# Optimization experiments

Hardware: AMD Instinct MI355X
Metric: run time of the kernel (lower is better)

The kernel has to match this reference:

```python
import jax, jax.numpy as jnp
import numpy as np

N = 10000   # nodes
E = 320000  # directed edges (self-loops added inside reference, per PyG default)
H1, C = 4, 128  # gat1: 4 heads x 128; gat2: 1 head x 128
NEG_SLOPE = 0.2


def _glorot(k, shape):
    lim = float(np.sqrt(6.0 / (shape[0] + shape[-1])))
    return jax.random.uniform(k, shape, jnp.float32, -lim, lim)


def setup_inputs() -> dict:
    key = jax.random.key(0)
    ks = jax.random.split(key, 12)
    x = jax.random.normal(ks[0], (N, 2), jnp.float32)
    edge_index = jax.random.randint(ks[1], (2, E), 0, N, dtype=jnp.int32).astype(jnp.int64)
    W1 = _glorot(ks[2], (2, H1 * C))
    att_src1 = _glorot(ks[3], (H1, C))
    att_dst1 = _glorot(ks[4], (H1, C))
    b1 = jnp.zeros((H1 * C,), jnp.float32)
    W2 = _glorot(ks[5], (H1 * C, C))
    att_src2 = _glorot(ks[6], (1, C))
    att_dst2 = _glorot(ks[7], (1, C))
    b2 = jnp.zeros((C,), jnp.float32)
    Wp = _glorot(ks[8], (C, 1))
    bp = jnp.zeros((1,), jnp.float32)
    return dict(x=x, edge_index=edge_index, W1=W1, att_src1=att_src1, att_dst1=att_dst1,
                b1=b1, W2=W2, att_src2=att_src2, att_dst2=att_dst2, b2=b2, Wp=Wp, bp=bp)


def _gat_conv(x, src, dst, W, a_src, a_dst, b, heads, ch, concat):
    n = x.shape[0]
    h = (x @ W).reshape(n, heads, ch)                         # [N,H,C]
    # per-node attention halves, gathered per edge
    e = jax.nn.leaky_relu((h * a_src).sum(-1)[src] + (h * a_dst).sum(-1)[dst],
                          NEG_SLOPE)                           # [E,H]
    # segment softmax over incoming edges of each destination node
    m = jax.ops.segment_max(e, dst, num_segments=n)            # [N,H]
    p = jnp.exp(e - m[dst])
    s = jax.ops.segment_sum(p, dst, num_segments=n)
    alpha = p / (s[dst] + 1e-16)                               # [E,H]
    out = jax.ops.segment_sum(h[src] * alpha[..., None], dst, num_segments=n)  # [N,H,C]
    out = out.reshape(n, heads * ch) if concat else out.mean(axis=1)
    return out + b


def reference(x, edge_index, W1, att_src1, att_dst1, b1, W2, att_src2, att_dst2, b2, Wp, bp):
    n = x.shape[0]
    loop = jnp.arange(n, dtype=edge_index.dtype)               # PyG add_self_loops=True
    src = jnp.concatenate([edge_index[0], loop])
    dst = jnp.concatenate([edge_index[1], loop])
    h = jax.nn.relu(_gat_conv(x, src, dst, W1, att_src1, att_dst1, b1, H1, C, True))
    h = jax.nn.relu(_gat_conv(h, src, dst, W2, att_src2, att_dst2, b2, 1, C, True))
    logits = h @ Wp + bp                                       # [N,1]
    return logits.squeeze(-1)
```

## Files before the change

### kernel.cpp

```cpp
#include <hip/hip_runtime.h>
#include <hip/hip_fp16.h>
#include <math.h>

#define N_NODES 10000
#define E_IN    320000
#define E_TOT   330000
#define H1      4
#define C       128
#define F1      512

typedef _Float16 f16x8 __attribute__((ext_vector_type(8)));
typedef float    f32x4 __attribute__((ext_vector_type(4)));

__global__ __launch_bounds__(256) void k_as1z(
    const float* __restrict__ x, const float* __restrict__ W1,
    const float* __restrict__ asw, const float* __restrict__ adw,
    float4* __restrict__ as1v, float4* __restrict__ ad1v, int* __restrict__ deg)
{
    __shared__ float red[4][8];
    __shared__ float prep_s[16];
    int tid = threadIdx.x;
    {
        int j = tid;
        int j2 = tid + 256;
        float w0a = W1[j],  w1a = W1[F1 + j];
        float w0b = W1[j2], w1b = W1[F1 + j2];
        float aa = asw[j], dd = adw[j], ab = asw[j2], db = adw[j2];
        float q0 = w0a*aa, q1 = w1a*aa, q2 = w0a*dd, q3 = w1a*dd;
        float q4 = w0b*ab, q5 = w1b*ab, q6 = w0b*db, q7 = w1b*db;
        #pragma unroll
        for (int o = 32; o > 0; o >>= 1) {
            q0 += __shfl_down(q0, o); q1 += __shfl_down(q1, o);
            q2 += __shfl_down(q2, o); q3 += __shfl_down(q3, o);
            q4 += __shfl_down(q4, o); q5 += __shfl_down(q5, o);
            q6 += __shfl_down(q6, o); q7 += __shfl_down(q7, o);
        }
        int wave = tid >> 6, lane = tid & 63;
        if (lane == 0) {
            red[wave][0] = q0; red[wave][1] = q1; red[wave][2] = q2; red[wave][3] = q3;
            red[wave][4] = q4; red[wave][5] = q5; red[wave][6] = q6; red[wave][7] = q7;
        }
        __syncthreads();
        if (tid < 16) {
            int t = tid >> 2;
            int h = tid & 3;
            int w0 = (h & 1) * 2;
            int r  = t + (h >> 1) * 4;
            prep_s[t*4 + h] = red[w0][r] + red[w0+1][r];
        }
        __syncthreads();
    }
    int n = blockIdx.x * 256 + tid;
    if (n >= N_NODES) return;
    deg[n] = 0;
    float x0 = x[2*n], x1 = x[2*n+1];
    float4 A0 = *(const float4*)(prep_s);
    float4 A1 = *(const float4*)(prep_s + 4);
    float4 D0 = *(const float4*)(prep_s + 8);
    float4 D1 = *(const float4*)(prep_s + 12);
    as1v[n] = make_float4(x0*A0.x + x1*A1.x, x0*A0.y + x1*A1.y,
                          x0*A0.z + x1*A1.z, x0*A0.w + x1*A1.w);
    ad1v[n] = make_float4(x0*D0.x + x1*D1.x, x0*D0.y + x1*D1.y,
                          x0*D0.z + x1*D1.z, x0*D0.w + x1*D1.w);
}

__global__ __launch_bounds__(256) void k_w2cvt(
    const float* __restrict__ W2, _Float16* __restrict__ w2h)
{
    int t = blockIdx.x * 256 + threadIdx.x;
    int e0 = t * 4;
    int c = e0 >> 9;
    int kk0 = e0 & 511;
    int xr = (c & 7) << 3;
    _Float16 o[4];
    #pragma unroll
    for (int j = 0; j < 4; ++j) {
        int k = (kk0 + j) ^ xr;
        o[j] = (_Float16)W2[k * C + c];
    }
    *(uint2*)(w2h + c * F1 + kk0) = *(uint2*)o;
}

__global__ void k_hist(const int* __restrict__ dsti, int* __restrict__ deg) {
    int t = blockIdx.x * blockDim.x + threadIdx.x;
    if (t >= E_TOT) return;
    int d = (t < E_IN) ? dsti[t] : (t - E_IN);
    atomicAdd(&deg[d], 1);
}

__global__ __launch_bounds__(256) void k_scan(
    const int* __restrict__ deg, int* __restrict__ offs, int* __restrict__ cursor)
{
    __shared__ int part[256];
    int tid = threadIdx.x;
    const int CH = (N_NODES + 255) / 256;
    int start = tid * CH;
    int sum = 0;
    for (int i = 0; i < CH; ++i) { int idx = start + i; if (idx < N_NODES) sum += deg[idx]; }
    part[tid] = sum;
    __syncthreads();
    for (int off = 1; off < 256; off <<= 1) {
        int v = (tid >= off) ? part[tid - off] : 0;
        __syncthreads();
        part[tid] += v;
        __syncthreads();
    }
    int base = (tid == 0) ? 0 : part[tid - 1];
    for (int i = 0; i < CH; ++i) {
        int idx = start + i;
        if (idx < N_NODES) { offs[idx] = base; cursor[idx] = base; base += deg[idx]; }
    }
    if (tid == 255) offs[N_NODES] = base;
}

__global__ void k_scatter(const int* __restrict__ srci, const int* __restrict__ dsti,
                          int* __restrict__ cursor, int* __restrict__ scsr) {
    int t = blockIdx.x * blockDim.x + threadIdx.x;
    if (t >= E_TOT) return;
    int d = (t < E_IN) ? dsti[t] : (t - E_IN);
    int s = (t < E_IN) ? srci[t] : (t - E_IN);
    int pos = atomicAdd(&cursor[d], 1);
    scsr[pos] = s;
}

__global__ __launch_bounds__(256) void k_fused1(
    const int* __restrict__ offs, const int* __restrict__ scsr,
    const float4* __restrict__ as1v, const float4* __restrict__ ad1v,
    const float2* __restrict__ xv, float* __restrict__ wxn)
{
    int node = blockIdx.x * 16 + (threadIdx.x >> 4);
    int sub = threadIdx.x & 15;
    int beg = offs[node], end = offs[node + 1];
    float4 ad = ad1v[node];
    float s0 = 0.f, s1 = 0.f, s2 = 0.f, s3 = 0.f;
    float w00 = 0.f, w01 = 0.f, w10 = 0.f, w11 = 0.f;
    float w20 = 0.f, w21 = 0.f, w30 = 0.f, w31 = 0.f;
    int i = beg + sub;
    if (i < end) {
        int s = scsr[i];
        for (;;) {
            float4 a = as1v[s];
            float2 xs = xv[s];
            int inext = i + 16;
            bool more = inext < end;
            int snext = 0;
            if (more) snext = scsr[inext];
            float e0 = a.x + ad.x; e0 = e0 > 0.f ? e0 : 0.2f*e0;
            float e1 = a.y + ad.y; e1 = e1 > 0.f ? e1 : 0.2f*e1;
            float e2 = a.z + ad.z; e2 = e2 > 0.f ? e2 : 0.2f*e2;
            float e3 = a.w + ad.w; e3 = e3 > 0.f ? e3 : 0.2f*e3;
            float p0 = __expf(e0), p1 = __expf(e1), p2 = __expf(e2), p3 = __expf(e3);
            s0 += p0; s1 += p1; s2 += p2; s3 += p3;
            w00 += p0*xs.x; w01 += p0*xs.y; w10 += p1*xs.x; w11 += p1*xs.y;
            w20 += p2*xs.x; w21 += p2*xs.y; w30 += p3*xs.x; w31 += p3*xs.y;
            if (!more) break;
            i = inext; s = snext;
        }
    }
    #pragma unroll
    for (int o = 1; o < 16; o <<= 1) {
        s0 += __shfl_xor(s0, o); s1 += __shfl_xor(s1, o);
        s2 += __shfl_xor(s2, o); s3 += __shfl_xor(s3, o);
        w00 += __shfl_xor(w00, o); w01 += __shfl_xor(w01, o);
        w10 += __shfl_xor(w10, o); w11 += __shfl_xor(w11, o);
        w20 += __shfl_xor(w20, o); w21 += __shfl_xor(w21, o);
        w30 += __shfl_xor(w30, o); w31 += __shfl_xor(w31, o);
    }
    if (sub == 0) {
        float i0 = 1.f/(s0 + 1e-16f), i1 = 1.f/(s1 + 1e-16f);
        float i2 = 1.f/(s2 + 1e-16f), i3 = 1.f/(s3 + 1e-16f);
        float4* W = (float4*)(wxn + node*8);
        W[0] = make_float4(w00*i0, w01*i0, w10*i1, w11*i1);
        W[1] = make_float4(w20*i2, w21*i2, w30*i3, w31*i3);
    }
}

__global__ __launch_bounds__(256, 1) void k_gemm2(
    const float* __restrict__ wxn, const float* __restrict__ W1,
    const float* __restrict__ b1, const _Float16* __restrict__ w2h,
    const float* __restrict__ asw, const float* __restrict__ adw,
    __half* __restrict__ h2h, float* __restrict__ as2, float* __restrict__ ad2)
{
    __shared__ _Float16 w2t[F1 * C];
    int tid = threadIdx.x;
    #pragma unroll
    for (int it = 0; it < 32; ++it) {
        int idx = (it * 256 + tid) * 8;
        *(f16x8*)(w2t + idx) = *(const f16x8*)(w2h + idx);
    }
    __syncthreads();

    int wid = tid >> 6, lane = tid & 63;
    int tile = blockIdx.x * 4 + wid;
    if (tile >= N_NODES / 16) return;
    int n0w = tile * 16;
    int col = lane & 15;
    int krow = (lane >> 4) * 8;
    int qr4 = (lane >> 4) * 4;
    int node = n0w + col;

    float4 wv0 = *(const float4*)(wxn + node * 8);
    float4 wv1 = *(const float4*)(wxn + node * 8 + 4);

    f32x4 acc[8];
    #pragma unroll
    for (int mt = 0; mt < 8; ++mt) acc[mt] = (f32x4){0.f, 0.f, 0.f, 0.f};

    int xr = (col & 7) << 3;
    const float* W1r0 = W1;
    const float* W1r1 = W1 + F1;

    #pragma unroll
    for (int h = 0; h < 4; ++h) {
        float wa = (h == 0) ? wv0.x : (h == 1) ? wv0.z : (h == 2) ? wv1.x : wv1.z;
        float wb = (h == 0) ? wv0.y : (h == 1) ? wv0.w : (h == 2) ? wv1.y : wv1.w;
        #pragma unroll
        for (int kq = 0; kq < 4; ++kq) {
            int kc = h * 4 + kq;
            int k0 = kc * 32 + krow;
            float4 a0 = *(const float4*)(W1r0 + k0);
            float4 a1 = *(const float4*)(W1r0 + k0 + 4);
            float4 c0 = *(const float4*)(W1r1 + k0);
            float4 c1 = *(const float4*)(W1r1 + k0 + 4);
            float4 b0 = *(const float4*)(b1 + k0);
            float4 b1v = *(const float4*)(b1 + k0 + 4);
            f16x8 bf;
            float v;
            v = wa*a0.x + wb*c0.x + b0.x;  bf[0] = (_Float16)(v > 0.f ? v : 0.f);
            v = wa*a0.y + wb*c0.y + b0.y;  bf[1] = (_Float16)(v > 0.f ? v : 0.f);
            v = wa*a0.z + wb*c0.z + b0.z;  bf[2] = (_Float16)(v > 0.f ? v : 0.f);
            v = wa*a0.w + wb*c0.w + b0.w;  bf[3] = (_Float16)(v > 0.f ? v : 0.f);
            v = wa*a1.x + wb*c1.x + b1v.x; bf[4] = (_Float16)(v > 0.f ? v : 0.f);
            v = wa*a1.y + wb*c1.y + b1v.y; bf[5] = (_Float16)(v > 0.f ? v : 0.f);
            v = wa*a1.z + wb*c1.z + b1v.z; bf[6] = (_Float16)(v > 0.f ? v : 0.f);
            v = wa*a1.w + wb*c1.w + b1v.w; bf[7] = (_Float16)(v > 0.f ? v : 0.f);
            int kbase = col * F1 + (k0 ^ xr);
            #pragma unroll
            for (int mt = 0; mt < 8; ++mt) {
                f16x8 af = *(const f16x8*)(&w2t[mt * 16 * F1 + kbase]);
                acc[mt] = __builtin_amdgcn_mfma_f32_16x16x32_f16(af, bf, acc[mt], 0, 0, 0);
            }
        }
    }

    float ps = 0.f, pd = 0.f;
    __half* hbase = h2h + (size_t)node * C + qr4;
    #pragma unroll
    for (int mt = 0; mt < 8; ++mt) {
        f32x4 a = acc[mt];
        __half2 lo = __floats2half2_rn(a[0], a[1]);
        __half2 hi = __floats2half2_rn(a[2], a[3]);
        uint2 u; u.x = *(uint*)&lo; u.y = *(uint*)&hi;
        *(uint2*)(hbase + mt * 16) = u;
        float4 av = *(const float4*)(asw + mt * 16 + qr4);
        float4 dv = *(const float4*)(adw + mt * 16 + qr4);
        ps += a[0]*av.x + a[1]*av.y + a[2]*av.z + a[3]*av.w;
        pd += a[0]*dv.x + a[1]*dv.y + a[2]*dv.z + a[3]*dv.w;
    }
    ps += __shfl_xor(ps, 16); ps += __shfl_xor(ps, 32);
    pd += __shfl_xor(pd, 16); pd += __shfl_xor(pd, 32);
    if (lane < 16) { as2[n0w + lane] = ps; ad2[n0w + lane] = pd; }
}

__global__ __launch_bounds__(256) void k_agg2(
    const int* __restrict__ offs, const int* __restrict__ scsr,
    const float* __restrict__ as2, const float* __restrict__ ad2,
    const __half* __restrict__ h2h, const float* __restrict__ b2,
    const float* __restrict__ Wp, const float* __restrict__ bp,
    float* __restrict__ out)
{
    int n = blockIdx.x * 4 + (threadIdx.x >> 6);
    int lane = threadIdx.x & 63;
    int half = lane >> 5;
    int cl = lane & 31;
    int beg = offs[n], end = offs[n + 1];
    float adn = ad2[n];
    float a0 = 0.f, a1 = 0.f, a2 = 0.f, a3 = 0.f, psum = 0.f;
    int i = beg + half;
    for (; i + 6 < end; i += 8) {
        int s0 = scsr[i], s1 = scsr[i+2], s2 = scsr[i+4], s3 = scsr[i+6];
        float e0 = as2[s0] + adn, e1 = as2[s1] + adn;
        float e2 = as2[s2] + adn, e3 = as2[s3] + adn;
        uint2 q0 = *(const uint2*)(h2h + (size_t)s0*C + 4*cl);
        uint2 q1 = *(const uint2*)(h2h + (size_t)s1*C + 4*cl);
        uint2 q2 = *(const uint2*)(h2h + (size_t)s2*C + 4*cl);
        uint2 q3 = *(const uint2*)(h2h + (size_t)s3*C + 4*cl);
        e0 = e0 > 0.f ? e0 : 0.2f*e0;  float p0 = __expf(e0);
        e1 = e1 > 0.f ? e1 : 0.2f*e1;  float p1 = __expf(e1);
        e2 = e2 > 0.f ? e2 : 0.2f*e2;  float p2 = __expf(e2);
        e3 = e3 > 0.f ? e3 : 0.2f*e3;  float p3 = __expf(e3);
        psum += (p0 + p1) + (p2 + p3);
        float2 f0a = __half22float2(*(__half2*)&q0.x), f0b = __half22float2(*(__half2*)&q0.y);
        float2 f1a = __half22float2(*(__half2*)&q1.x), f1b = __half22float2(*(__half2*)&q1.y);
        float2 f2a = __half22float2(*(__half2*)&q2.x), f2b = __half22float2(*(__half2*)&q2.y);
        float2 f3a = __half22float2(*(__half2*)&q3.x), f3b = __half22float2(*(__half2*)&q3.y);
        a0 += p0*f0a.x + p1*f1a.x + p2*f2a.x + p3*f3a.x;
        a1 += p0*f0a.y + p1*f1a.y + p2*f2a.y + p3*f3a.y;
        a2 += p0*f0b.x + p1*f1b.x + p2*f2b.x + p3*f3b.x;
        a3 += p0*f0b.y + p1*f1b.y + p2*f2b.y + p3*f3b.y;
    }
    for (; i < end; i += 2) {
        int s = scsr[i];
        float e = as2[s] + adn; e = e > 0.f ? e : 0.2f*e;
        float p = __expf(e);
        psum += p;
        uint2 q = *(const uint2*)(h2h + (size_t)s*C + 4*cl);
        float2 fa = __half22float2(*(__half2*)&q.x), fb = __half22float2(*(__half2*)&q.y);
        a0 += p*fa.x; a1 += p*fa.y; a2 += p*fb.x; a3 += p*fb.y;
    }
    a0 += __shfl_xor(a0, 32); a1 += __shfl_xor(a1, 32);
    a2 += __shfl_xor(a2, 32); a3 += __shfl_xor(a3, 32);
    psum += __shfl_xor(psum, 32);
    float inv = 1.f / (psum + 1e-16f);
    float4 bb = *(const float4*)(b2 + 4*cl);
    float4 wp = *(const float4*)(Wp + 4*cl);
    float v0 = a0*inv + bb.x; v0 = v0 > 0.f ? v0 : 0.f;
    float v1 = a1*inv + bb.y; v1 = v1 > 0.f ? v1 : 0.f;
    float v2 = a2*inv + bb.z; v2 = v2 > 0.f ? v2 : 0.f;
    float v3 = a3*inv + bb.w; v3 = v3 > 0.f ? v3 : 0.f;
    float contrib = v0*wp.x + v1*wp.y + v2*wp.z + v3*wp.w;
    #pragma unroll
    for (int o = 1; o < 32; o <<= 1) contrib += __shfl_xor(contrib, o);
    if (lane == 0) out[n] = contrib + bp[0];
}

extern "C" void kernel_launch(void* const* d_in, const int* in_sizes, int n_in,
                              void* d_out, int out_size, void* d_ws, size_t ws_size,
                              hipStream_t stream)
{
    const float* x    = (const float*)d_in[0];
    const int*   ei   = (const int*)d_in[1];
    const int*   srci = ei;
    const int*   dsti = ei + E_IN;
    const float* W1   = (const float*)d_in[2];
    const float* as1w = (const float*)d_in[3];
    const float* ad1w = (const float*)d_in[4];
    const float* b1   = (const float*)d_in[5];
    const float* W2   = (const float*)d_in[6];
    const float* as2w = (const float*)d_in[7];
    const float* ad2w = (const float*)d_in[8];
    const float* b2   = (const float*)d_in[9];
    const float* Wp   = (const float*)d_in[10];
    const float* bp   = (const float*)d_in[11];
    float* out = (float*)d_out;

    char* ws = (char*)d_ws;
    size_t off = 0;
    auto alloc = [&](size_t bytes) -> char* {
        char* p = ws + off;
        off = (off + bytes + 255) & ~(size_t)255;
        return p;
    };
    float4*    as1v   = (float4*)alloc((size_t)N_NODES * 16);
    float4*    ad1v   = (float4*)alloc((size_t)N_NODES * 16);
    float*     wxn    = (float*)alloc((size_t)N_NODES * 8 * 4);
    __half*    h2h    = (__half*)alloc((size_t)N_NODES * C * 2);
    _Float16*  w2h    = (_Float16*)alloc((size_t)F1 * C * 2);
    float*     as2    = (float*)alloc((size_t)N_NODES * 4);
    float*     ad2    = (float*)alloc((size_t)N_NODES * 4);
    int*       deg    = (int*)alloc((size_t)N_NODES * 4);
    int*       offs   = (int*)alloc((size_t)(N_NODES + 1) * 4);
    int*       cursor = (int*)alloc((size_t)N_NODES * 4);
    int*       scsr   = (int*)alloc((size_t)E_TOT * 4);

    const int EB = 256;
    const int egrid = (E_TOT + EB - 1) / EB;
    const int ngrid = (N_NODES + 255) / 256;

    k_as1z<<<ngrid, 256, 0, stream>>>(x, W1, as1w, ad1w, as1v, ad1v, deg);
    k_w2cvt<<<64, 256, 0, stream>>>(W2, w2h);
    k_hist<<<egrid, EB, 0, stream>>>(dsti, deg);
    k_scan<<<1, 256, 0, stream>>>(deg, offs, cursor);
    k_scatter<<<egrid, EB, 0, stream>>>(srci, dsti, cursor, scsr);
    k_fused1<<<N_NODES / 16, 256, 0, stream>>>(offs, scsr, as1v, ad1v,
                                               (const float2*)x, wxn);
    k_gemm2<<<(N_NODES/16 + 3) / 4, 256, 0, stream>>>(wxn, W1, b1, w2h, as2w, ad2w,
                                                      h2h, as2, ad2);
    k_agg2<<<N_NODES / 4, 256, 0, stream>>>(offs, scsr, as2, ad2, h2h, b2, Wp, bp, out);
}
```

Measured before the change: 185.8 us.

## Fuse CSR build and layer-1 aggregation into one cooperative persistent kernel

Replaces six separate launches (prep, W2 convert, histogram, scan, scatter, layer-1 aggregate) with a single cooperative kernel of 512 blocks that separates the phases with grid.sync(). The single-block scan becomes a two-level parallel scan: 40 blocks each scan their chunk, then one thread combines the block sums. The aim is to cut kernel launch overhead and the serial scan bottleneck. In exchange it adds six grid-wide barriers, and the grid-stride loops run on a fixed 512-block grid that depends on cooperative residency.

```diff
diff --git a/kernel.cpp b/kernel.cpp
--- a/kernel.cpp
+++ b/kernel.cpp
@@ -1,6 +1,9 @@
 #include <hip/hip_runtime.h>
+#include <hip/hip_cooperative_groups.h>
 #include <hip/hip_fp16.h>
 #include <math.h>
+
+namespace cg = cooperative_groups;
 
 #define N_NODES 10000
 #define E_IN    320000
@@ -8,21 +11,29 @@
 #define H1      4
 #define C       128
 #define F1      512
+#define GB      512
 
 typedef _Float16 f16x8 __attribute__((ext_vector_type(8)));
 typedef float    f32x4 __attribute__((ext_vector_type(4)));
 
-__global__ __launch_bounds__(256) void k_as1z(
-    const float* __restrict__ x, const float* __restrict__ W1,
-    const float* __restrict__ asw, const float* __restrict__ adw,
-    float4* __restrict__ as1v, float4* __restrict__ ad1v, int* __restrict__ deg)
+__global__ __launch_bounds__(256, 2) void k_build(
+    const float* __restrict__ x, const int* __restrict__ srci, const int* __restrict__ dsti,
+    const float* __restrict__ W1, const float* __restrict__ asw, const float* __restrict__ adw,
+    const float* __restrict__ W2, _Float16* __restrict__ w2h,
+    float4* __restrict__ as1v, float4* __restrict__ ad1v,
+    int* __restrict__ deg, int* __restrict__ offs, int* __restrict__ cursor,
+    int* __restrict__ scsr, int* __restrict__ exclg, int* __restrict__ bsum,
+    float* __restrict__ wxn)
 {
+    cg::grid_group grid = cg::this_grid();
     __shared__ float red[4][8];
     __shared__ float prep_s[16];
+    __shared__ int sc[256];
     int tid = threadIdx.x;
-    {
-        int j = tid;
-        int j2 = tid + 256;
+    int b = blockIdx.x;
+
+    if (b < 40) {
+        int j = tid, j2 = tid + 256;
         float w0a = W1[j],  w1a = W1[F1 + j];
         float w0b = W1[j2], w1b = W1[F1 + j2];
         float aa = asw[j], dd = adw[j], ab = asw[j2], db = adw[j2];
@@ -49,129 +60,122 @@
             prep_s[t*4 + h] = red[w0][r] + red[w0+1][r];
         }
         __syncthreads();
-    }
-    int n = blockIdx.x * 256 + tid;
-    if (n >= N_NODES) return;
-    deg[n] = 0;
-    float x0 = x[2*n], x1 = x[2*n+1];
-    float4 A0 = *(const float4*)(prep_s);
-    float4 A1 = *(const float4*)(prep_s + 4);
-    float4 D0 = *(const float4*)(prep_s + 8);
-    float4 D1 = *(const float4*)(prep_s + 12);
-    as1v[n] = make_float4(x0*A0.x + x1*A1.x, x0*A0.y + x1*A1.y,
-                          x0*A0.z + x1*A1.z, x0*A0.w + x1*A1.w);
-    ad1v[n] = make_float4(x0*D0.x + x1*D1.x, x0*D0.y + x1*D1.y,
-                          x0*D0.z + x1*D1.z, x0*D0.w + x1*D1.w);
-}
-
-__global__ __launch_bounds__(256) void k_w2cvt(
-    const float* __restrict__ W2, _Float16* __restrict__ w2h)
-{
-    int t = blockIdx.x * 256 + threadIdx.x;
-    int e0 = t * 4;
-    int c = e0 >> 9;
-    int kk0 = e0 & 511;
-    int xr = (c & 7) << 3;
-    _Float16 o[4];
-    #pragma unroll
-    for (int j = 0; j < 4; ++j) {
-        int k = (kk0 + j) ^ xr;
-        o[j] = (_Float16)W2[k * C + c];
-    }
-    *(uint2*)(w2h + c * F1 + kk0) = *(uint2*)o;
-}
-
-__global__ void k_hist(const int* __restrict__ dsti, int* __restrict__ deg) {
-    int t = blockIdx.x * blockDim.x + threadIdx.x;
-    if (t >= E_TOT) return;
-    int d = (t < E_IN) ? dsti[t] : (t - E_IN);
-    atomicAdd(&deg[d], 1);
-}
-
-__global__ __launch_bounds__(256) void k_scan(
-    const int* __restrict__ deg, int* __restrict__ offs, int* __restrict__ cursor)
-{
-    __shared__ int part[256];
-    int tid = threadIdx.x;
-    const int CH = (N_NODES + 255) / 256;
-    int start = tid * CH;
-    int sum = 0;
-    for (int i = 0; i < CH; ++i) { int idx = start + i; if (idx < N_NODES) sum += deg[idx]; }
-    part[tid] = sum;
-    __syncthreads();
-    for (int off = 1; off < 256; off <<= 1) {
-        int v = (tid >= off) ? part[tid - off] : 0;
+        int n = b * 256 + tid;
+        if (n < N_NODES) {
+            deg[n] = 0;
+            float x0 = x[2*n], x1 = x[2*n+1];
+            float4 A0 = *(const float4*)(prep_s);
+            float4 A1 = *(const float4*)(prep_s + 4);
+            float4 D0 = *(const float4*)(prep_s + 8);
+            float4 D1 = *(const float4*)(prep_s + 12);
+            as1v[n] = make_float4(x0*A0.x + x1*A1.x, x0*A0.y + x1*A1.y,
+                                  x0*A0.z + x1*A1.z, x0*A0.w + x1*A1.w);
+            ad1v[n] = make_float4(x0*D0.x + x1*D1.x, x0*D0.y + x1*D1.y,
+                                  x0*D0.z + x1*D1.z, x0*D0.w + x1*D1.w);
+        }
+    } else if (b < 104) {
+        int t = (b - 40) * 256 + tid;
+        int e0 = t * 4;
+        int c = e0 >> 9;
+        int kk0 = e0 & 511;
+        int xr = (c & 7) << 3;
+        _Float16 o4[4];
+        #pragma unroll
+        for (int j = 0; j < 4; ++j) o4[j] = (_Float16)W2[((kk0 + j) ^ xr) * C + c];
+        *(uint2*)(w2h + c * F1 + kk0) = *(uint2*)o4;
+    }
+    grid.sync();
+
+    for (int t = b * 256 + tid; t < E_TOT; t += GB * 256) {
+        int d = (t < E_IN) ? dsti[t] : (t - E_IN);
+        atomicAdd(&deg[d], 1);
+    }
+    grid.sync();
+
+    int n2 = b * 256 + tid;
+    if (b < 40) {
+        int v = (n2 < N_NODES) ? deg[n2] : 0;
+        sc[tid] = v;
         __syncthreads();
-        part[tid] += v;
-        __syncthreads();
-    }
-    int base = (tid == 0) ? 0 : part[tid - 1];
-    for (int i = 0; i < CH; ++i) {
-        int idx = start + i;
-        if (idx < N_NODES) { offs[idx] = base; cursor[idx] = base; base += deg[idx]; }
-    }
-    if (tid == 255) offs[N_NODES] = base;
-}
-
-__global__ void k_scatter(const int* __restrict__ srci, const int* __restrict__ dsti,
-                          int* __restrict__ cursor, int* __restrict__ scsr) {
-    int t = blockIdx.x * blockDim.x + threadIdx.x;
-    if (t >= E_TOT) return;
-    int d = (t < E_IN) ? dsti[t] : (t - E_IN);
-    int s = (t < E_IN) ? srci[t] : (t - E_IN);
-    int pos = atomicAdd(&cursor[d], 1);
-    scsr[pos] = s;
-}
-
-__global__ __launch_bounds__(256) void k_fused1(
-    const int* __restrict__ offs, const int* __restrict__ scsr,
-    const float4* __restrict__ as1v, const float4* __restrict__ ad1v,
-    const float2* __restrict__ xv, float* __restrict__ wxn)
-{
-    int node = blockIdx.x * 16 + (threadIdx.x >> 4);
-    int sub = threadIdx.x & 15;
-    int beg = offs[node], end = offs[node + 1];
-    float4 ad = ad1v[node];
-    float s0 = 0.f, s1 = 0.f, s2 = 0.f, s3 = 0.f;
-    float w00 = 0.f, w01 = 0.f, w10 = 0.f, w11 = 0.f;
-    float w20 = 0.f, w21 = 0.f, w30 = 0.f, w31 = 0.f;
-    int i = beg + sub;
-    if (i < end) {
-        int s = scsr[i];
-        for (;;) {
-            float4 a = as1v[s];
-            float2 xs = xv[s];
-            int inext = i + 16;
-            bool more = inext < end;
-            int snext = 0;
-            if (more) snext = scsr[inext];
-            float e0 = a.x + ad.x; e0 = e0 > 0.f ? e0 : 0.2f*e0;
-            float e1 = a.y + ad.y; e1 = e1 > 0.f ? e1 : 0.2f*e1;
-            float e2 = a.z + ad.z; e2 = e2 > 0.f ? e2 : 0.2f*e2;
-            float e3 = a.w + ad.w; e3 = e3 > 0.f ? e3 : 0.2f*e3;
-            float p0 = __expf(e0), p1 = __expf(e1), p2 = __expf(e2), p3 = __expf(e3);
-            s0 += p0; s1 += p1; s2 += p2; s3 += p3;
-            w00 += p0*xs.x; w01 += p0*xs.y; w10 += p1*xs.x; w11 += p1*xs.y;
-            w20 += p2*xs.x; w21 += p2*xs.y; w30 += p3*xs.x; w31 += p3*xs.y;
-            if (!more) break;
-            i = inext; s = snext;
-        }
-    }
-    #pragma unroll
-    for (int o = 1; o < 16; o <<= 1) {
-        s0 += __shfl_xor(s0, o); s1 += __shfl_xor(s1, o);
-        s2 += __shfl_xor(s2, o); s3 += __shfl_xor(s3, o);
-        w00 += __shfl_xor(w00, o); w01 += __shfl_xor(w01, o);
-        w10 += __shfl_xor(w10, o); w11 += __shfl_xor(w11, o);
-        w20 += __shfl_xor(w20, o); w21 += __shfl_xor(w21, o);
-        w30 += __shfl_xor(w30, o); w31 += __shfl_xor(w31, o);
-    }
-    if (sub == 0) {
-        float i0 = 1.f/(s0 + 1e-16f), i1 = 1.f/(s1 + 1e-16f);
-        float i2 = 1.f/(s2 + 1e-16f), i3 = 1.f/(s3 + 1e-16f);
-        float4* W = (float4*)(wxn + node*8);
-        W[0] = make_float4(w00*i0, w01*i0, w10*i1, w11*i1);
-        W[1] = make_float4(w20*i2, w21*i2, w30*i3, w31*i3);
+        for (int o = 1; o < 256; o <<= 1) {
+            int u = (tid >= o) ? sc[tid - o] : 0;
+            __syncthreads();
+            sc[tid] += u;
+            __syncthreads();
+        }
+        if (n2 < N_NODES) exclg[n2] = sc[tid] - v;
+        if (tid == 255) bsum[b] = sc[255];
+    }
+    grid.sync();
+
+    if (b == 0 && tid == 0) {
+        int run = 0;
+        for (int i = 0; i < 40; ++i) { int s = bsum[i]; bsum[i] = run; run += s; }
+        offs[N_NODES] = run;
+    }
+    grid.sync();
+
+    if (b < 40 && n2 < N_NODES) {
+        int o = bsum[b] + exclg[n2];
+        offs[n2] = o;
+        cursor[n2] = o;
+    }
+    grid.sync();
+
+    for (int t = b * 256 + tid; t < E_TOT; t += GB * 256) {
+        int d = (t < E_IN) ? dsti[t] : (t - E_IN);
+        int s = (t < E_IN) ? srci[t] : (t - E_IN);
+        int pos = atomicAdd(&cursor[d], 1);
+        scsr[pos] = s;
+    }
+    grid.sync();
+
+    const float2* xv = (const float2*)x;
+    int sub = tid & 15;
+    for (int node = b * 16 + (tid >> 4); node < N_NODES; node += GB * 16) {
+        int beg = offs[node], end = offs[node + 1];
+        float4 ad = ad1v[node];
+        float s0 = 0.f, s1 = 0.f, s2 = 0.f, s3 = 0.f;
+        float w00 = 0.f, w01 = 0.f, w10 = 0.f, w11 = 0.f;
+        float w20 = 0.f, w21 = 0.f, w30 = 0.f, w31 = 0.f;
+        int i = beg + sub;
+        if (i < end) {
+            int s = scsr[i];
+            for (;;) {
+                float4 a = as1v[s];
+                float2 xs = xv[s];
+                int inext = i + 16;
+                bool more = inext < end;
+                int snext = 0;
+                if (more) snext = scsr[inext];
+                float e0 = a.x + ad.x; e0 = e0 > 0.f ? e0 : 0.2f*e0;
+                float e1 = a.y + ad.y; e1 = e1 > 0.f ? e1 : 0.2f*e1;
+                float e2 = a.z + ad.z; e2 = e2 > 0.f ? e2 : 0.2f*e2;
+                float e3 = a.w + ad.w; e3 = e3 > 0.f ? e3 : 0.2f*e3;
+                float p0 = __expf(e0), p1 = __expf(e1), p2 = __expf(e2), p3 = __expf(e3);
+                s0 += p0; s1 += p1; s2 += p2; s3 += p3;
+                w00 += p0*xs.x; w01 += p0*xs.y; w10 += p1*xs.x; w11 += p1*xs.y;
+                w20 += p2*xs.x; w21 += p2*xs.y; w30 += p3*xs.x; w31 += p3*xs.y;
+                if (!more) break;
+                i = inext; s = snext;
+            }
+        }
+        #pragma unroll
+        for (int o = 1; o < 16; o <<= 1) {
+            s0 += __shfl_xor(s0, o); s1 += __shfl_xor(s1, o);
+            s2 += __shfl_xor(s2, o); s3 += __shfl_xor(s3, o);
+            w00 += __shfl_xor(w00, o); w01 += __shfl_xor(w01, o);
+            w10 += __shfl_xor(w10, o); w11 += __shfl_xor(w11, o);
+            w20 += __shfl_xor(w20, o); w21 += __shfl_xor(w21, o);
+            w30 += __shfl_xor(w30, o); w31 += __shfl_xor(w31, o);
+        }
+        if (sub == 0) {
+            float i0 = 1.f/(s0 + 1e-16f), i1 = 1.f/(s1 + 1e-16f);
+            float i2 = 1.f/(s2 + 1e-16f), i3 = 1.f/(s3 + 1e-16f);
+            float4* W = (float4*)(wxn + node*8);
+            W[0] = make_float4(w00*i0, w01*i0, w10*i1, w11*i1);
+            W[1] = make_float4(w20*i2, w21*i2, w30*i3, w31*i3);
+        }
     }
 }
 
@@ -362,18 +366,20 @@
     int*       offs   = (int*)alloc((size_t)(N_NODES + 1) * 4);
     int*       cursor = (int*)alloc((size_t)N_NODES * 4);
     int*       scsr   = (int*)alloc((size_t)E_TOT * 4);
-
-    const int EB = 256;
-    const int egrid = (E_TOT + EB - 1) / EB;
-    const int ngrid = (N_NODES + 255) / 256;
-
-    k_as1z<<<ngrid, 256, 0, stream>>>(x, W1, as1w, ad1w, as1v, ad1v, deg);
-    k_w2cvt<<<64, 256, 0, stream>>>(W2, w2h);
-    k_hist<<<egrid, EB, 0, stream>>>(dsti, deg);
-    k_scan<<<1, 256, 0, stream>>>(deg, offs, cursor);
-    k_scatter<<<egrid, EB, 0, stream>>>(srci, dsti, cursor, scsr);
-    k_fused1<<<N_NODES / 16, 256, 0, stream>>>(offs, scsr, as1v, ad1v,
-                                               (const float2*)x, wxn);
+    int*       exclg  = (int*)alloc((size_t)N_NODES * 4);
+    int*       bsum   = (int*)alloc(64 * 4);
+
+    void* kargs[] = {
+        (void*)&x, (void*)&srci, (void*)&dsti,
+        (void*)&W1, (void*)&as1w, (void*)&ad1w,
+        (void*)&W2, (void*)&w2h,
+        (void*)&as1v, (void*)&ad1v,
+        (void*)&deg, (void*)&offs, (void*)&cursor,
+        (void*)&scsr, (void*)&exclg, (void*)&bsum,
+        (void*)&wxn
+    };
+    hipLaunchCooperativeKernel((void*)k_build, dim3(GB), dim3(256), kargs, 0, stream);
+
     k_gemm2<<<(N_NODES/16 + 3) / 4, 256, 0, stream>>>(wxn, W1, b1, w2h, as2w, ad2w,
                                                       h2h, as2, ad2);
     k_agg2<<<N_NODES / 4, 256, 0, stream>>>(offs, scsr, as2, ad2, h2h, b2, Wp, bp, out);
```

New measurement: 507.6 us. +173.1%, slower.

## Merge W2 conversion into prep kernel, interleave node attrs, LDS-staged scan

Applied to the files above, without the earlier changes.

Folds the W2 fp16 conversion into the first prep kernel as extra blocks, removing one launch. Packs the per-node source attention and x coordinates into one 32-byte record so each edge gather in the first aggregation touches a single cache line. Rewrites the single-block scan to stage degrees in LDS and reuse the local prefix, avoiding re-reading degrees from global memory. This uses 40KB of LDS in the scan block and extra bytes per node record.

```diff
diff --git a/kernel.cpp b/kernel.cpp
--- a/kernel.cpp
+++ b/kernel.cpp
@@ -15,14 +15,27 @@
 __global__ __launch_bounds__(256) void k_as1z(
     const float* __restrict__ x, const float* __restrict__ W1,
     const float* __restrict__ asw, const float* __restrict__ adw,
-    float4* __restrict__ as1v, float4* __restrict__ ad1v, int* __restrict__ deg)
-{
+    const float* __restrict__ W2, _Float16* __restrict__ w2h,
+    float* __restrict__ a1x, float4* __restrict__ ad1v, int* __restrict__ deg)
+{
+    int tid = threadIdx.x;
+    int b = blockIdx.x;
+    if (b >= 40) {
+        int t = (b - 40) * 256 + tid;
+        int e0 = t * 4;
+        int c = e0 >> 9;
+        int kk0 = e0 & 511;
+        int xr = (c & 7) << 3;
+        _Float16 o4[4];
+        #pragma unroll
+        for (int j = 0; j < 4; ++j) o4[j] = (_Float16)W2[((kk0 + j) ^ xr) * C + c];
+        *(uint2*)(w2h + c * F1 + kk0) = *(uint2*)o4;
+        return;
+    }
     __shared__ float red[4][8];
     __shared__ float prep_s[16];
-    int tid = threadIdx.x;
     {
-        int j = tid;
-        int j2 = tid + 256;
+        int j = tid, j2 = tid + 256;
         float w0a = W1[j],  w1a = W1[F1 + j];
         float w0b = W1[j2], w1b = W1[F1 + j2];
         float aa = asw[j], dd = adw[j], ab = asw[j2], db = adw[j2];
@@ -50,7 +63,7 @@
         }
         __syncthreads();
     }
-    int n = blockIdx.x * 256 + tid;
+    int n = b * 256 + tid;
     if (n >= N_NODES) return;
     deg[n] = 0;
     float x0 = x[2*n], x1 = x[2*n+1];
@@ -58,27 +71,12 @@
     float4 A1 = *(const float4*)(prep_s + 4);
     float4 D0 = *(const float4*)(prep_s + 8);
     float4 D1 = *(const float4*)(prep_s + 12);
-    as1v[n] = make_float4(x0*A0.x + x1*A1.x, x0*A0.y + x1*A1.y,
-                          x0*A0.z + x1*A1.z, x0*A0.w + x1*A1.w);
+    float4* A = (float4*)(a1x + n * 8);
+    A[0] = make_float4(x0*A0.x + x1*A1.x, x0*A0.y + x1*A1.y,
+                       x0*A0.z + x1*A1.z, x0*A0.w + x1*A1.w);
+    A[1] = make_float4(x0, x1, 0.f, 0.f);
     ad1v[n] = make_float4(x0*D0.x + x1*D1.x, x0*D0.y + x1*D1.y,
                           x0*D0.z + x1*D1.z, x0*D0.w + x1*D1.w);
-}
-
-__global__ __launch_bounds__(256) void k_w2cvt(
-    const float* __restrict__ W2, _Float16* __restrict__ w2h)
-{
-    int t = blockIdx.x * 256 + threadIdx.x;
-    int e0 = t * 4;
-    int c = e0 >> 9;
-    int kk0 = e0 & 511;
-    int xr = (c & 7) << 3;
-    _Float16 o[4];
-    #pragma unroll
-    for (int j = 0; j < 4; ++j) {
-        int k = (kk0 + j) ^ xr;
-        o[j] = (_Float16)W2[k * C + c];
-    }
-    *(uint2*)(w2h + c * F1 + kk0) = *(uint2*)o;
 }
 
 __global__ void k_hist(const int* __restrict__ dsti, int* __restrict__ deg) {
@@ -91,26 +89,39 @@
 __global__ __launch_bounds__(256) void k_scan(
     const int* __restrict__ deg, int* __restrict__ offs, int* __restrict__ cursor)
 {
-    __shared__ int part[256];
+    __shared__ int lds[10240];
+    __shared__ int sc[256];
     int tid = threadIdx.x;
-    const int CH = (N_NODES + 255) / 256;
-    int start = tid * CH;
+    for (int i = tid; i < 10240; i += 256) lds[i] = (i < N_NODES) ? deg[i] : 0;
+    __syncthreads();
+    const int CH = 40;
+    int base = tid * CH;
     int sum = 0;
-    for (int i = 0; i < CH; ++i) { int idx = start + i; if (idx < N_NODES) sum += deg[idx]; }
-    part[tid] = sum;
+    #pragma unroll 8
+    for (int j = 0; j < CH; ++j) {
+        int v = lds[base + j];
+        lds[base + j] = sum;
+        sum += v;
+    }
+    sc[tid] = sum;
     __syncthreads();
-    for (int off = 1; off < 256; off <<= 1) {
-        int v = (tid >= off) ? part[tid - off] : 0;
+    for (int o = 1; o < 256; o <<= 1) {
+        int u = (tid >= o) ? sc[tid - o] : 0;
         __syncthreads();
-        part[tid] += v;
+        sc[tid] += u;
         __syncthreads();
     }
-    int base = (tid == 0) ? 0 : part[tid - 1];
-    for (int i = 0; i < CH; ++i) {
-        int idx = start + i;
-        if (idx < N_NODES) { offs[idx] = base; cursor[idx] = base; base += deg[idx]; }
-    }
-    if (tid == 255) offs[N_NODES] = base;
+    int chunk_off = (tid == 0) ? 0 : sc[tid - 1];
+    #pragma unroll 8
+    for (int j = 0; j < CH; ++j) {
+        int idx = base + j;
+        if (idx < N_NODES) {
+            int o = lds[idx] + chunk_off;
+            offs[idx] = o;
+            cursor[idx] = o;
+        }
+    }
+    if (tid == 255) offs[N_NODES] = sc[255];
 }
 
 __global__ void k_scatter(const int* __restrict__ srci, const int* __restrict__ dsti,
@@ -125,8 +136,8 @@
 
 __global__ __launch_bounds__(256) void k_fused1(
     const int* __restrict__ offs, const int* __restrict__ scsr,
-    const float4* __restrict__ as1v, const float4* __restrict__ ad1v,
-    const float2* __restrict__ xv, float* __restrict__ wxn)
+    const float* __restrict__ a1x, const float4* __restrict__ ad1v,
+    float* __restrict__ wxn)
 {
     int node = blockIdx.x * 16 + (threadIdx.x >> 4);
     int sub = threadIdx.x & 15;
@@ -139,8 +150,8 @@
     if (i < end) {
         int s = scsr[i];
         for (;;) {
-            float4 a = as1v[s];
-            float2 xs = xv[s];
+            float4 a  = *(const float4*)(a1x + s * 8);
+            float2 xs = *(const float2*)(a1x + s * 8 + 4);
             int inext = i + 16;
             bool more = inext < end;
             int snext = 0;
@@ -351,7 +362,7 @@
         off = (off + bytes + 255) & ~(size_t)255;
         return p;
     };
-    float4*    as1v   = (float4*)alloc((size_t)N_NODES * 16);
+    float*     a1x    = (float*)alloc((size_t)N_NODES * 8 * 4);
     float4*    ad1v   = (float4*)alloc((size_t)N_NODES * 16);
     float*     wxn    = (float*)alloc((size_t)N_NODES * 8 * 4);
     __half*    h2h    = (__half*)alloc((size_t)N_NODES * C * 2);
@@ -365,15 +376,12 @@
 
     const int EB = 256;
     const int egrid = (E_TOT + EB - 1) / EB;
-    const int ngrid = (N_NODES + 255) / 256;
-
-    k_as1z<<<ngrid, 256, 0, stream>>>(x, W1, as1w, ad1w, as1v, ad1v, deg);
-    k_w2cvt<<<64, 256, 0, stream>>>(W2, w2h);
+
+    k_as1z<<<104, 256, 0, stream>>>(x, W1, as1w, ad1w, W2, w2h, a1x, ad1v, deg);
     k_hist<<<egrid, EB, 0, stream>>>(dsti, deg);
     k_scan<<<1, 256, 0, stream>>>(deg, offs, cursor);
     k_scatter<<<egrid, EB, 0, stream>>>(srci, dsti, cursor, scsr);
-    k_fused1<<<N_NODES / 16, 256, 0, stream>>>(offs, scsr, as1v, ad1v,
-                                               (const float2*)x, wxn);
+    k_fused1<<<N_NODES / 16, 256, 0, stream>>>(offs, scsr, a1x, ad1v, wxn);
     k_gemm2<<<(N_NODES/16 + 3) / 4, 256, 0, stream>>>(wxn, W1, b1, w2h, as2w, ad2w,
                                                       h2h, as2, ad2);
     k_agg2<<<N_NODES / 4, 256, 0, stream>>>(offs, scsr, as2, ad2, h2h, b2, Wp, bp, out);
```

Result: faster. 178.6 us (-3.9%).
